# Performance work log

Measured on AMD Instinct MI355X. Metric: run time of the kernel, lower is better.

The kernel has to match this reference:

```python
import jax, jax.numpy as jnp
import numpy as np

HEAD_N = 16
EMBED_D = 1024
MASK_FILL = 1e-09  # source uses masked_fill(mask==0, 1e-09), NOT -inf


def setup_inputs() -> dict:
    key = jax.random.key(0)
    ks = jax.random.split(key, 8)
    B, S, D = 4, 4096, EMBED_D
    L = S // HEAD_N
    q = jax.random.normal(ks[0], (B, S, D), dtype=jnp.float32)
    k = jax.random.normal(ks[1], (B, S, D), dtype=jnp.float32)
    v = jax.random.normal(ks[2], (B, S, D), dtype=jnp.float32)
    mask = jax.random.randint(ks[3], (B, L, L), 0, 2, dtype=jnp.int32)
    scale = 0.02
    Wq = jax.random.normal(ks[4], (D, D), dtype=jnp.float32) * scale
    Wk = jax.random.normal(ks[5], (D, D), dtype=jnp.float32) * scale
    Wv = jax.random.normal(ks[6], (D, D), dtype=jnp.float32) * scale
    Wo = jax.random.normal(ks[7], (D, D), dtype=jnp.float32) * scale
    return {"q": q, "k": k, "v": v, "mask": mask, "Wq": Wq, "Wk": Wk, "Wv": Wv, "Wo": Wo}


def _split_heads(x, B):
    # Faithful to source bug: view(B, -1, head_n, embedding_d).transpose(1, 2)
    # -> splits the SEQUENCE dim by head_n; per-head dim stays EMBED_D.
    return x.reshape(B, -1, HEAD_N, EMBED_D).transpose(0, 2, 1, 3)  # [B,h,L,D]


def reference(q, k, v, mask, Wq, Wk, Wv, Wo):
    B, S, D = q.shape
    qh = _split_heads(q @ Wq, B)
    kh = _split_heads(k @ Wk, B)
    vh = _split_heads(v @ Wv, B)
    # score: [B, h, L, L], L = S // head_n
    score = jnp.einsum("bhld,bhmd->bhlm", qh, kh) / jnp.sqrt(jnp.float32(D))
    m = mask[:, None, :, :]  # unsqueeze(1) -> broadcast over heads
    score = jnp.where(m == 0, jnp.float32(MASK_FILL), score)
    att = jax.nn.softmax(score, axis=-1)  # dropout p=0.0 -> identity
    x = jnp.einsum("bhlm,bhmd->bhld", att, vh)  # [B,h,L,D]
    x = x.transpose(0, 2, 1, 3).reshape(B, S, D)
    return x @ Wo
```

## Files before the change

### kernel.cpp

```cpp
#include <hip/hip_runtime.h>
#include <hip/hip_bf16.h>

typedef __bf16 bf16x8 __attribute__((ext_vector_type(8)));
typedef float f32x4 __attribute__((ext_vector_type(4)));
typedef unsigned short ushort_t;
typedef unsigned int uint_t;

#define HN 16
#define LSEQ 256
#define DD 1024
#define BB 4
#define SS 4096
#define MROWS (BB * SS)
#define BHN (BB * HN)

__device__ __forceinline__ ushort_t f2bf(float f) {
  uint_t u = __builtin_bit_cast(uint_t, f);
  u += 0x7fffu + ((u >> 16) & 1u);
  return (ushort_t)(u >> 16);
}
__device__ __forceinline__ uint_t pk2(float lo, float hi) {
  return (uint_t)f2bf(lo) | ((uint_t)f2bf(hi) << 16);
}

__global__ __launch_bounds__(256) void cvt3(const float4* __restrict__ s0,
                                            const float4* __restrict__ s1,
                                            const float4* __restrict__ s2,
                                            uint4* __restrict__ out) {
  const int z = blockIdx.y;
  const float4* in = (z == 0) ? s0 : (z == 1) ? s1 : s2;
  const long i = (long)blockIdx.x * 256 + threadIdx.x;
  const float4 a = in[i * 2];
  const float4 b = in[i * 2 + 1];
  uint4 o;
  o.x = pk2(a.x, a.y);
  o.y = pk2(a.z, a.w);
  o.z = pk2(b.x, b.y);
  o.w = pk2(b.z, b.w);
  out[(long)z * 2097152 + i] = o;
}

__global__ __launch_bounds__(256) void transpose_w4(const float* __restrict__ W0,
                                                    const float* __restrict__ W1,
                                                    const float* __restrict__ W2,
                                                    const float* __restrict__ W3,
                                                    ushort_t* __restrict__ WT) {
  __shared__ float tile[32][33];
  const int z = blockIdx.z;
  const float* W = (z == 0) ? W0 : (z == 1) ? W1 : (z == 2) ? W2 : W3;
  ushort_t* dst = WT + (long)z * 1048576;
  const int tx = threadIdx.x, ty = threadIdx.y;
  const int bn = blockIdx.x * 32, bk = blockIdx.y * 32;
#pragma unroll
  for (int j = 0; j < 32; j += 8)
    tile[ty + j][tx] = W[(long)(bk + ty + j) * DD + bn + tx];
  __syncthreads();
#pragma unroll
  for (int j = 0; j < 32; j += 8)
    dst[(long)(bn + ty + j) * DD + bk + tx] = f2bf(tile[tx][ty + j]);
}

__global__ __launch_bounds__(256) void transpose_v(const ushort_t* __restrict__ vh,
                                                   ushort_t* __restrict__ vhT) {
  __shared__ ushort_t tile[32][33];
  const int tx = threadIdx.x, ty = threadIdx.y;
  const long zo = (long)blockIdx.z * (LSEQ * DD);
  const ushort_t* src = vh + zo;
  ushort_t* dst = vhT + zo;
  const int bd = blockIdx.x * 32;
  const int bl = blockIdx.y * 32;
#pragma unroll
  for (int j = 0; j < 32; j += 8)
    tile[ty + j][tx] = src[(long)(bl + ty + j) * DD + bd + tx];
  __syncthreads();
#pragma unroll
  for (int j = 0; j < 32; j += 8)
    dst[(long)(bd + ty + j) * LSEQ + bl + tx] = tile[tx][ty + j];
}

__global__ __launch_bounds__(256, 2) void score_sm(const ushort_t* __restrict__ qh,
                                                   const ushort_t* __restrict__ kh,
                                                   const int* __restrict__ mask,
                                                   ushort_t* __restrict__ att) {
  __shared__ char smemraw[81920];
  ushort_t* sA = (ushort_t*)smemraw;
  ushort_t* sB = (ushort_t*)(smemraw + 16384);
  float* Sf = (float*)smemraw;

  const int orig = blockIdx.x;
  const int wgid = (orig & 7) * 32 + (orig >> 3);
  const int bh = wgid >> 2, rb = wgid & 3;
  const int b = bh >> 4;
  const ushort_t* A = qh + ((long)bh * 256 + rb * 64) * 1024;
  const ushort_t* Bk = kh + (long)bh * 256 * 1024;

  const int t = threadIdx.x, lane = t & 63, wid = t >> 6;
  const int fr = lane & 15, q = lane >> 4;
  const int wc = wid * 64;
  const int sw0 = (q ^ (fr & 7)) * 8;
  const int sw1 = ((4 + q) ^ (fr & 7)) * 8;

  int srcAo[2], dstA[2], srcBo[8], dstB[8];
#pragma unroll
  for (int i = 0; i < 2; ++i) {
    const int c = i * 256 + t, row = c >> 3, gc = (c & 7) ^ (row & 7);
    srcAo[i] = row * 1024 + gc * 8;
    dstA[i] = (i * 256 + (t & 192)) * 8;
  }
#pragma unroll
  for (int i = 0; i < 8; ++i) {
    const int c = i * 256 + t, row = c >> 3, gc = (c & 7) ^ (row & 7);
    srcBo[i] = row * 1024 + gc * 8;
    dstB[i] = (i * 256 + (t & 192)) * 8;
  }

  auto stage = [&](int buf, int kt) {
    const int ko = kt * 64;
#pragma unroll
    for (int i = 0; i < 2; ++i)
      __builtin_amdgcn_global_load_lds(
          (const __attribute__((address_space(1))) void*)(A + srcAo[i] + ko),
          (__attribute__((address_space(3))) void*)(sA + buf * 4096 + dstA[i]), 16, 0, 0);
#pragma unroll
    for (int i = 0; i < 8; ++i)
      __builtin_amdgcn_global_load_lds(
          (const __attribute__((address_space(1))) void*)(Bk + srcBo[i] + ko),
          (__attribute__((address_space(3))) void*)(sB + buf * 16384 + dstB[i]), 16, 0, 0);
  };

  f32x4 acc[4][4];
#pragma unroll
  for (int m = 0; m < 4; ++m)
#pragma unroll
    for (int n = 0; n < 4; ++n) acc[m][n] = (f32x4){0.f, 0.f, 0.f, 0.f};

  stage(0, 0);
  __syncthreads();
  int cur = 0;
  for (int kt = 0; kt < 16; ++kt) {
    if (kt < 15) stage(cur ^ 1, kt + 1);
    bf16x8 af[4][2], bfv[4][2];
    const ushort_t* bA = sA + cur * 4096;
    const ushort_t* bB = sB + cur * 16384;
#pragma unroll
    for (int m = 0; m < 4; ++m) {
      af[m][0] = *(const bf16x8*)(bA + (m * 16 + fr) * 64 + sw0);
      af[m][1] = *(const bf16x8*)(bA + (m * 16 + fr) * 64 + sw1);
    }
#pragma unroll
    for (int n = 0; n < 4; ++n) {
      bfv[n][0] = *(const bf16x8*)(bB + (wc + n * 16 + fr) * 64 + sw0);
      bfv[n][1] = *(const bf16x8*)(bB + (wc + n * 16 + fr) * 64 + sw1);
    }
#pragma unroll
    for (int m = 0; m < 4; ++m)
#pragma unroll
      for (int n = 0; n < 4; ++n) {
        acc[m][n] = __builtin_amdgcn_mfma_f32_16x16x32_bf16(af[m][0], bfv[n][0], acc[m][n], 0, 0, 0);
        acc[m][n] = __builtin_amdgcn_mfma_f32_16x16x32_bf16(af[m][1], bfv[n][1], acc[m][n], 0, 0, 0);
      }
    __syncthreads();
    cur ^= 1;
  }

#pragma unroll
  for (int m = 0; m < 4; ++m)
#pragma unroll
    for (int n = 0; n < 4; ++n)
#pragma unroll
      for (int r = 0; r < 4; ++r)
        Sf[(m * 16 + q * 4 + r) * 256 + wc + n * 16 + fr] = acc[m][n][r];
  __syncthreads();

#pragma unroll 2
  for (int i = 0; i < 16; ++i) {
    const int row = wid * 16 + i;
    const int gl = rb * 64 + row;
    const f32x4 sv = *(const f32x4*)&Sf[row * 256 + lane * 4];
    const int4 mv = *(const int4*)&mask[((long)b * 256 + gl) * 256 + lane * 4];
    float s[4];
    s[0] = (mv.x == 0) ? 1e-9f : sv[0] * 0.03125f;
    s[1] = (mv.y == 0) ? 1e-9f : sv[1] * 0.03125f;
    s[2] = (mv.z == 0) ? 1e-9f : sv[2] * 0.03125f;
    s[3] = (mv.w == 0) ? 1e-9f : sv[3] * 0.03125f;
    float mx = fmaxf(fmaxf(s[0], s[1]), fmaxf(s[2], s[3]));
#pragma unroll
    for (int off = 32; off; off >>= 1) mx = fmaxf(mx, __shfl_xor(mx, off));
    float e[4], sum = 0.f;
#pragma unroll
    for (int j = 0; j < 4; ++j) {
      e[j] = __expf(s[j] - mx);
      sum += e[j];
    }
#pragma unroll
    for (int off = 32; off; off >>= 1) sum += __shfl_xor(sum, off);
    const float inv = 1.0f / sum;
    ushort4 o;
    o.x = f2bf(e[0] * inv);
    o.y = f2bf(e[1] * inv);
    o.z = f2bf(e[2] * inv);
    o.w = f2bf(e[3] * inv);
    *(ushort4*)&att[((long)bh * 256 + gl) * 256 + lane * 4] = o;
  }
}

__global__ __launch_bounds__(256, 2) void gemm_tn(const ushort_t* __restrict__ Ab,
                                                  const ushort_t* __restrict__ Btp,
                                                  void* __restrict__ Cp, int K, int ldA,
                                                  int ldB, int ldC, long batchA,
                                                  long batchB, long batchC) {
  __shared__ ushort_t smem[16384];
  ushort_t* sA = smem;
  ushort_t* sB = smem + 8192;

  const int bx = blockIdx.x, by = blockIdx.y, z = blockIdx.z;
  const int rowBase = by * 128;
  const int colBase = bx * 128;

  const int t = threadIdx.x;
  const int lane = t & 63;
  const int wid = t >> 6;
  const int wr = (wid >> 1) * 64;
  const int wc = (wid & 1) * 64;
  const int fr = lane & 15;
  const int fk = (lane >> 4) * 8;

  const ushort_t* Atile = Ab + batchA * z + (long)rowBase * ldA;
  const ushort_t* Btile = Btp + batchB * z + (long)colBase * ldB;

  f32x4 acc[4][4];
#pragma unroll
  for (int m = 0; m < 4; ++m)
#pragma unroll
    for (int n = 0; n < 4; ++n) acc[m][n] = (f32x4){0.f, 0.f, 0.f, 0.f};

  const int NT = K >> 5;

  auto stageAB = [&](int buf, int kt) {
    const long ko = (long)kt * 32;
#pragma unroll
    for (int i = 0; i < 2; ++i) {
      const int c = i * 256 + t;
      const int cw = i * 256 + (t & 192);
      __builtin_amdgcn_global_load_lds(
          (const __attribute__((address_space(1))) void*)(Atile + (long)(c >> 2) * ldA + ko +
                                                          (c & 3) * 8),
          (__attribute__((address_space(3))) void*)(sA + buf * 4096 + cw * 8), 16, 0, 0);
      __builtin_amdgcn_global_load_lds(
          (const __attribute__((address_space(1))) void*)(Btile + (long)(c >> 2) * ldB + ko +
                                                          (c & 3) * 8),
          (__attribute__((address_space(3))) void*)(sB + buf * 4096 + cw * 8), 16, 0, 0);
    }
  };

  stageAB(0, 0);
  __syncthreads();

  int cur = 0;
  for (int kt = 0; kt < NT; ++kt) {
    if (kt + 1 < NT) stageAB(cur ^ 1, kt + 1);

    bf16x8 af[4], bfv[4];
    const ushort_t* baseA = sA + cur * 4096 + fk;
    const ushort_t* baseB = sB + cur * 4096 + fk;
#pragma unroll
    for (int m = 0; m < 4; ++m) af[m] = *(const bf16x8*)(baseA + (wr + m * 16 + fr) * 32);
#pragma unroll
    for (int n = 0; n < 4; ++n) bfv[n] = *(const bf16x8*)(baseB + (wc + n * 16 + fr) * 32);

#pragma unroll
    for (int m = 0; m < 4; ++m)
#pragma unroll
      for (int n = 0; n < 4; ++n)
        acc[m][n] = __builtin_amdgcn_mfma_f32_16x16x32_bf16(af[m], bfv[n], acc[m][n], 0, 0, 0);

    __syncthreads();
    cur ^= 1;
  }

  const int rq = (lane >> 4) * 4;
#pragma unroll
  for (int m = 0; m < 4; ++m)
#pragma unroll
    for (int n = 0; n < 4; ++n)
#pragma unroll
      for (int r = 0; r < 4; ++r)
        smem[(wr + m * 16 + rq + r) * 128 + wc + n * 16 + fr] = f2bf(acc[m][n][r]);
  __syncthreads();
  ushort_t* Cb = (ushort_t*)Cp;
  const int c8 = (lane & 15) * 8;
#pragma unroll
  for (int i = 0; i < 8; ++i) {
    const int row = i * 16 + wid * 4 + (lane >> 4);
    const uint4 val = *(const uint4*)(smem + row * 128 + c8);
    const int l = rowBase + row;
    const int orow = ((z >> 4) << 12) + l * 16 + (z & 15);
    *(uint4*)(Cb + (long)orow * 1024 + colBase + c8) = val;
  }
}

#define SBAR() asm volatile("s_barrier" ::: "memory")
#define LGKM0() asm volatile("s_waitcnt lgkmcnt(0)" ::: "memory")
#define VM(N) asm volatile("s_waitcnt vmcnt(" #N ")" ::: "memory")

template <int SMODE>
__global__ __launch_bounds__(512, 1) void gemm256(const ushort_t* __restrict__ A0,
                                                  const ushort_t* __restrict__ A1,
                                                  const ushort_t* __restrict__ A2,
                                                  const ushort_t* __restrict__ Btp,
                                                  void* __restrict__ Cp, long bStrideZ,
                                                  long cStrideZ) {
  __shared__ ushort_t sm[65536];

  const int orig = blockIdx.x;
  const int cpx = (int)gridDim.x >> 3;
  const int wgid = (orig & 7) * cpx + (orig >> 3);
  const int z = wgid >> 8;
  const int tile = wgid & 255;
  const int by = tile >> 2, bx = tile & 3;
  const int rowBase = by * 256, colBase = bx * 256;

  const ushort_t* Ab = (z == 0) ? A0 : (z == 1) ? A1 : A2;
  const ushort_t* Bt = Btp + bStrideZ * z;

  const int t = threadIdx.x;
  const int lane = t & 63;
  const int wid = t >> 6;
  const int wm = wid >> 2;
  const int wn = wid & 3;
  const int fr = lane & 15;
  const int q = lane >> 4;

  const int sw0 = ((q ^ (fr & 7)) * 8);
  const int sw1 = (((4 + q) ^ (fr & 7)) * 8);
  const int aoff0 = fr * 64 + sw0;
  const int aoff1 = fr * 64 + sw1;
  const int bbase = ((wn & 1) * 64 + fr) * 64;
  const int boff0 = bbase + sw0;
  const int boff1 = bbase + sw1;

  const ushort_t* srcA[2][2];
  const ushort_t* srcB[2][2];
  int ldsoff[2];
#pragma unroll
  for (int i = 0; i < 2; ++i) {
    const int c = i * 512 + t;
    const int rowc = c >> 3;
    const int gc = (c & 7) ^ (rowc & 7);
    srcA[0][i] = Ab + (long)(rowBase + rowc) * 1024 + gc * 8;
    srcA[1][i] = Ab + (long)(rowBase + 128 + rowc) * 1024 + gc * 8;
    srcB[0][i] = Bt + (long)(colBase + rowc) * 1024 + gc * 8;
    srcB[1][i] = Bt + (long)(colBase + 128 + rowc) * 1024 + gc * 8;
    ldsoff[i] = (c & ~63) * 8;
  }

#define STAGE(kind, h, T)                                                                   \
  do {                                                                                      \
    ushort_t* _d = sm + ((kind) ? 32768 : 0) + ((T) & 1) * 16384 + (h) * 8192;              \
    const ushort_t* _s0 = ((kind) ? srcB[h][0] : srcA[h][0]) + (long)(T) * 64;              \
    __builtin_amdgcn_global_load_lds((const __attribute__((address_space(1))) void*)_s0,    \
                                     (__attribute__((address_space(3))) void*)(_d + ldsoff[0]), \
                                     16, 0, 0);                                             \
    const ushort_t* _s1 = ((kind) ? srcB[h][1] : srcA[h][1]) + (long)(T) * 64;              \
    __builtin_amdgcn_global_load_lds((const __attribute__((address_space(1))) void*)_s1,    \
                                     (__attribute__((address_space(3))) void*)(_d + ldsoff[1]), \
                                     16, 0, 0);                                             \
  } while (0)

  f32x4 acc[8][4];
#pragma unroll
  for (int m = 0; m < 8; ++m)
#pragma unroll
    for (int n = 0; n < 4; ++n) acc[m][n] = (f32x4){0.f, 0.f, 0.f, 0.f};

  bf16x8 af[4][2], bf0[2][2], bf1[2][2];

#define LDA4(dbuf, msub)                                                         \
  do {                                                                           \
    const ushort_t* _b = sm + (dbuf)*16384 + wm * 8192 + (msub)*4096;            \
    _Pragma("unroll") for (int m2 = 0; m2 < 4; ++m2) {                           \
      af[m2][0] = *(const bf16x8*)(_b + m2 * 1024 + aoff0);                      \
      af[m2][1] = *(const bf16x8*)(_b + m2 * 1024 + aoff1);                      \
    }                                                                            \
  } while (0)

#define LDB2(dbuf, nsub, bfv)                                                    \
  do {                                                                           \
    const ushort_t* _b = sm + 32768 + (dbuf)*16384 + (wn >> 1) * 8192 + (nsub)*2048; \
    _Pragma("unroll") for (int n2 = 0; n2 < 2; ++n2) {                           \
      bfv[n2][0] = *(const bf16x8*)(_b + n2 * 1024 + boff0);                     \
      bfv[n2][1] = *(const bf16x8*)(_b + n2 * 1024 + boff1);                     \
    }                                                                            \
  } while (0)

#define MMQ(msub, nsub, bfv)                                                     \
  do {                                                                           \
    _Pragma("unroll") for (int m2 = 0; m2 < 4; ++m2)                             \
        _Pragma("unroll") for (int n2 = 0; n2 < 2; ++n2) {                       \
      acc[(msub)*4 + m2][(nsub)*2 + n2] = __builtin_amdgcn_mfma_f32_16x16x32_bf16( \
          af[m2][0], bfv[n2][0], acc[(msub)*4 + m2][(nsub)*2 + n2], 0, 0, 0);    \
      acc[(msub)*4 + m2][(nsub)*2 + n2] = __builtin_amdgcn_mfma_f32_16x16x32_bf16( \
          af[m2][1], bfv[n2][1], acc[(msub)*4 + m2][(nsub)*2 + n2], 0, 0, 0);    \
    }                                                                            \
  } while (0)

#define PH_OPEN() SBAR(); LGKM0(); __builtin_amdgcn_s_setprio(1)
#define PH_CLOSE() __builtin_amdgcn_s_setprio(0); SBAR()

  const int NT = 16;
  const int NI = 8;

  STAGE(0, 0, 0);
  STAGE(0, 1, 0);
  STAGE(1, 0, 0);
  STAGE(1, 1, 0);
  STAGE(0, 0, 1);
  STAGE(0, 1, 1);
  STAGE(1, 0, 1);
  STAGE(1, 1, 1);
  VM(8);
  SBAR();

  for (int it = 0; it < NI - 1; ++it) {
    const int T0 = 2 * it;
    LDA4(0, 0);
    LDB2(0, 0, bf0);
    PH_OPEN(); MMQ(0, 0, bf0); PH_CLOSE();
    LDB2(0, 1, bf1);
    PH_OPEN(); MMQ(0, 1, bf1); PH_CLOSE();
    LDA4(0, 1);
    STAGE(1, 0, T0 + 2);
    STAGE(1, 1, T0 + 2);
    PH_OPEN(); MMQ(1, 1, bf1); PH_CLOSE();
    STAGE(0, 0, T0 + 2);
    STAGE(0, 1, T0 + 2);
    SBAR();
    __builtin_amdgcn_s_setprio(1);
    MMQ(1, 0, bf0);
    __builtin_amdgcn_s_setprio(0);
    VM(8);
    SBAR();
    LDA4(1, 0);
    LDB2(1, 0, bf0);
    PH_OPEN(); MMQ(0, 0, bf0); PH_CLOSE();
    LDB2(1, 1, bf1);
    PH_OPEN(); MMQ(0, 1, bf1); PH_CLOSE();
    LDA4(1, 1);
    STAGE(1, 0, T0 + 3);
    STAGE(1, 1, T0 + 3);
    PH_OPEN(); MMQ(1, 1, bf1); PH_CLOSE();
    STAGE(0, 0, T0 + 3);
    STAGE(0, 1, T0 + 3);
    SBAR();
    __builtin_amdgcn_s_setprio(1);
    MMQ(1, 0, bf0);
    __builtin_amdgcn_s_setprio(0);
    VM(8);
    SBAR();
  }

  {
    LDA4(0, 0);
    LDB2(0, 0, bf0);
    PH_OPEN(); MMQ(0, 0, bf0); PH_CLOSE();
    LDB2(0, 1, bf1);
    PH_OPEN(); MMQ(0, 1, bf1); PH_CLOSE();
    LDA4(0, 1);
    PH_OPEN(); MMQ(1, 1, bf1); PH_CLOSE();
    SBAR();
    __builtin_amdgcn_s_setprio(1);
    MMQ(1, 0, bf0);
    __builtin_amdgcn_s_setprio(0);
    VM(0);
    SBAR();
    LDA4(1, 0);
    LDB2(1, 0, bf0);
    PH_OPEN(); MMQ(0, 0, bf0); PH_CLOSE();
    LDB2(1, 1, bf1);
    PH_OPEN(); MMQ(0, 1, bf1); PH_CLOSE();
    LDA4(1, 1);
    PH_OPEN(); MMQ(1, 1, bf1); PH_CLOSE();
    SBAR();
    MMQ(1, 0, bf0);
    SBAR();
  }

  const int rq = q * 4;
  if constexpr (SMODE == 0) {
    float* Cf = (float*)Cp + cStrideZ * z;
#pragma unroll
    for (int m = 0; m < 8; ++m)
#pragma unroll
      for (int n = 0; n < 4; ++n)
#pragma unroll
        for (int r = 0; r < 4; ++r) {
          const int row = rowBase + wm * 128 + m * 16 + rq + r;
          const int col = colBase + wn * 64 + n * 16 + fr;
          Cf[(long)row * 1024 + col] = acc[m][n][r];
        }
  } else {
#pragma unroll
    for (int m = 0; m < 8; ++m)
#pragma unroll
      for (int n = 0; n < 4; ++n)
#pragma unroll
        for (int r = 0; r < 4; ++r) {
          const int row = wm * 128 + m * 16 + rq + r;
          const int col = wn * 64 + n * 16 + fr;
          sm[row * 256 + (((col >> 3) ^ (row & 7)) * 8) + (col & 7)] = f2bf(acc[m][n][r]);
        }
    __syncthreads();
    ushort_t* Cb = (ushort_t*)Cp + cStrideZ * z;
    const int cc = t & 31;
    const int r0 = t >> 5;
#pragma unroll
    for (int i = 0; i < 16; ++i) {
      const int row = r0 + i * 16;
      const uint4 val = *(const uint4*)(sm + row * 256 + ((cc ^ (row & 7)) * 8));
      const int grow = rowBase + row;
      const int b = grow >> 12;
      const int s = grow & 4095;
      const int orow = ((b << 4) + (s & 15)) * 256 + (s >> 4);
      *(uint4*)(Cb + (long)orow * 1024 + colBase + cc * 8) = val;
    }
  }
#undef STAGE
#undef LDA4
#undef LDB2
#undef MMQ
#undef PH_OPEN
#undef PH_CLOSE
}

extern "C" void kernel_launch(void* const* d_in, const int* in_sizes, int n_in,
                              void* d_out, int out_size, void* d_ws, size_t ws_size,
                              hipStream_t stream) {
  const float* q = (const float*)d_in[0];
  const float* k = (const float*)d_in[1];
  const float* v = (const float*)d_in[2];
  const int* mask = (const int*)d_in[3];
  const float* Wq = (const float*)d_in[4];
  const float* Wk = (const float*)d_in[5];
  const float* Wv = (const float*)d_in[6];
  const float* Wo = (const float*)d_in[7];
  float* out = (float*)d_out;

  char* ws = (char*)d_ws;
  const size_t MB = 1024 * 1024;
  ushort_t* WT = (ushort_t*)ws;
  const dim3 tb(32, 8);
  transpose_w4<<<dim3(32, 32, 4), tb, 0, stream>>>(Wq, Wk, Wv, Wo, WT);

  const bool big = ws_size >= (size_t)200 * MB;

  if (big) {
    ushort_t* qkvb = (ushort_t*)(ws + 8 * MB);
    ushort_t* qh = (ushort_t*)(ws + 104 * MB);
    ushort_t* kh = (ushort_t*)(ws + 136 * MB);
    ushort_t* vh = (ushort_t*)(ws + 168 * MB);
    ushort_t* vhT = (ushort_t*)(ws + 8 * MB);
    ushort_t* att = (ushort_t*)(ws + 40 * MB);
    ushort_t* x = (ushort_t*)(ws + 48 * MB);

    cvt3<<<dim3(8192, 3), 256, 0, stream>>>((const float4*)q, (const float4*)k,
                                            (const float4*)v, (uint4*)qkvb);
    gemm256<1><<<768, 512, 0, stream>>>(qkvb, qkvb + (size_t)16777216,
                                        qkvb + (size_t)33554432, WT, qh, 1 << 20,
                                        (long)16777216);
    transpose_v<<<dim3(32, 8, BHN), tb, 0, stream>>>(vh, vhT);
    score_sm<<<256, 256, 0, stream>>>(qh, kh, mask, att);
    gemm_tn<<<dim3(8, 2, BHN), 256, 0, stream>>>(att, vhT, x, 256, 256, 256, 1024,
                                                 (long)65536, (long)262144, 0);
    gemm256<0><<<256, 512, 0, stream>>>(x, x, x, WT + (size_t)3145728, out, 0, 0);
  } else {
    ushort_t* qb = (ushort_t*)(ws + 8 * MB);
    ushort_t* qh = (ushort_t*)(ws + 40 * MB);
    ushort_t* kh = (ushort_t*)(ws + 72 * MB);
    ushort_t* vh = (ushort_t*)(ws + 104 * MB);
    ushort_t* vhT = (ushort_t*)(ws + 136 * MB);
    ushort_t* att = (ushort_t*)(ws + 8 * MB);
    ushort_t* x = (ushort_t*)(ws + 16 * MB);

    cvt3<<<dim3(8192, 1), 256, 0, stream>>>((const float4*)q, (const float4*)q,
                                            (const float4*)q, (uint4*)qb);
    gemm256<1><<<256, 512, 0, stream>>>(qb, qb, qb, WT, qh, 0, 0);
    cvt3<<<dim3(8192, 1), 256, 0, stream>>>((const float4*)k, (const float4*)k,
                                            (const float4*)k, (uint4*)qb);
    gemm256<1><<<256, 512, 0, stream>>>(qb, qb, qb, WT + (size_t)1048576, kh, 0, 0);
    cvt3<<<dim3(8192, 1), 256, 0, stream>>>((const float4*)v, (const float4*)v,
                                            (const float4*)v, (uint4*)qb);
    gemm256<1><<<256, 512, 0, stream>>>(qb, qb, qb, WT + (size_t)2097152, vh, 0, 0);
    transpose_v<<<dim3(32, 8, BHN), tb, 0, stream>>>(vh, vhT);
    score_sm<<<256, 256, 0, stream>>>(qh, kh, mask, att);
    gemm_tn<<<dim3(8, 2, BHN), 256, 0, stream>>>(att, vhT, x, 256, 256, 256, 1024,
                                                 (long)65536, (long)262144, 0);
    gemm256<0><<<256, 512, 0, stream>>>(x, x, x, WT + (size_t)3145728, out, 0, 0);
  }
}
```

Baseline: 271.7 us.

## Fuse fp32-to-bf16 input conversion into the QKV projection GEMM

Removes the separate cvt3 pass that converted q, k and v to bf16. A new GEMM kernel instead loads fp32 A tiles straight into LDS and converts them to bf16 with v_cvt_pk_bf16_f32 while building MFMA fragments. This avoids writing and re-reading about 96MB of bf16 intermediates. In exchange, the A tiles take twice the LDS and global bandwidth per K step, the pipeline runs 32-wide K steps with a new schedule, and the small-workspace fallback path is dropped.

```diff
diff --git a/kernel.cpp b/kernel.cpp
--- a/kernel.cpp
+++ b/kernel.cpp
@@ -14,30 +14,18 @@
 #define MROWS (BB * SS)
 #define BHN (BB * HN)
 
+#define AS1 __attribute__((address_space(1)))
+#define AS3 __attribute__((address_space(3)))
+
 __device__ __forceinline__ ushort_t f2bf(float f) {
   uint_t u = __builtin_bit_cast(uint_t, f);
   u += 0x7fffu + ((u >> 16) & 1u);
   return (ushort_t)(u >> 16);
 }
-__device__ __forceinline__ uint_t pk2(float lo, float hi) {
-  return (uint_t)f2bf(lo) | ((uint_t)f2bf(hi) << 16);
-}
-
-__global__ __launch_bounds__(256) void cvt3(const float4* __restrict__ s0,
-                                            const float4* __restrict__ s1,
-                                            const float4* __restrict__ s2,
-                                            uint4* __restrict__ out) {
-  const int z = blockIdx.y;
-  const float4* in = (z == 0) ? s0 : (z == 1) ? s1 : s2;
-  const long i = (long)blockIdx.x * 256 + threadIdx.x;
-  const float4 a = in[i * 2];
-  const float4 b = in[i * 2 + 1];
-  uint4 o;
-  o.x = pk2(a.x, a.y);
-  o.y = pk2(a.z, a.w);
-  o.z = pk2(b.x, b.y);
-  o.w = pk2(b.z, b.w);
-  out[(long)z * 2097152 + i] = o;
+__device__ __forceinline__ uint_t cvtpk(float lo, float hi) {
+  uint_t r;
+  asm("v_cvt_pk_bf16_f32 %0, %1, %2" : "=v"(r) : "v"(lo), "v"(hi));
+  return r;
 }
 
 __global__ __launch_bounds__(256) void transpose_w4(const float* __restrict__ W0,
@@ -119,13 +107,13 @@
 #pragma unroll
     for (int i = 0; i < 2; ++i)
       __builtin_amdgcn_global_load_lds(
-          (const __attribute__((address_space(1))) void*)(A + srcAo[i] + ko),
-          (__attribute__((address_space(3))) void*)(sA + buf * 4096 + dstA[i]), 16, 0, 0);
+          (const AS1 void*)(A + srcAo[i] + ko),
+          (AS3 void*)(sA + buf * 4096 + dstA[i]), 16, 0, 0);
 #pragma unroll
     for (int i = 0; i < 8; ++i)
       __builtin_amdgcn_global_load_lds(
-          (const __attribute__((address_space(1))) void*)(Bk + srcBo[i] + ko),
-          (__attribute__((address_space(3))) void*)(sB + buf * 16384 + dstB[i]), 16, 0, 0);
+          (const AS1 void*)(Bk + srcBo[i] + ko),
+          (AS3 void*)(sB + buf * 16384 + dstB[i]), 16, 0, 0);
   };
 
   f32x4 acc[4][4];
@@ -243,13 +231,11 @@
       const int c = i * 256 + t;
       const int cw = i * 256 + (t & 192);
       __builtin_amdgcn_global_load_lds(
-          (const __attribute__((address_space(1))) void*)(Atile + (long)(c >> 2) * ldA + ko +
-                                                          (c & 3) * 8),
-          (__attribute__((address_space(3))) void*)(sA + buf * 4096 + cw * 8), 16, 0, 0);
+          (const AS1 void*)(Atile + (long)(c >> 2) * ldA + ko + (c & 3) * 8),
+          (AS3 void*)(sA + buf * 4096 + cw * 8), 16, 0, 0);
       __builtin_amdgcn_global_load_lds(
-          (const __attribute__((address_space(1))) void*)(Btile + (long)(c >> 2) * ldB + ko +
-                                                          (c & 3) * 8),
-          (__attribute__((address_space(3))) void*)(sB + buf * 4096 + cw * 8), 16, 0, 0);
+          (const AS1 void*)(Btile + (long)(c >> 2) * ldB + ko + (c & 3) * 8),
+          (AS3 void*)(sB + buf * 4096 + cw * 8), 16, 0, 0);
     }
   };
 
@@ -302,26 +288,23 @@
 #define SBAR() asm volatile("s_barrier" ::: "memory")
 #define LGKM0() asm volatile("s_waitcnt lgkmcnt(0)" ::: "memory")
 #define VM(N) asm volatile("s_waitcnt vmcnt(" #N ")" ::: "memory")
+#define PH_OPEN() SBAR(); LGKM0(); __builtin_amdgcn_s_setprio(1)
+#define PH_CLOSE() __builtin_amdgcn_s_setprio(0); SBAR()
 
 template <int SMODE>
 __global__ __launch_bounds__(512, 1) void gemm256(const ushort_t* __restrict__ A0,
-                                                  const ushort_t* __restrict__ A1,
-                                                  const ushort_t* __restrict__ A2,
                                                   const ushort_t* __restrict__ Btp,
-                                                  void* __restrict__ Cp, long bStrideZ,
-                                                  long cStrideZ) {
+                                                  void* __restrict__ Cp) {
   __shared__ ushort_t sm[65536];
 
   const int orig = blockIdx.x;
   const int cpx = (int)gridDim.x >> 3;
   const int wgid = (orig & 7) * cpx + (orig >> 3);
-  const int z = wgid >> 8;
-  const int tile = wgid & 255;
-  const int by = tile >> 2, bx = tile & 3;
+  const int by = wgid >> 2, bx = wgid & 3;
   const int rowBase = by * 256, colBase = bx * 256;
 
-  const ushort_t* Ab = (z == 0) ? A0 : (z == 1) ? A1 : A2;
-  const ushort_t* Bt = Btp + bStrideZ * z;
+  const ushort_t* Ab = A0;
+  const ushort_t* Bt = Btp;
 
   const int t = threadIdx.x;
   const int lane = t & 63;
@@ -358,13 +341,11 @@
   do {                                                                                      \
     ushort_t* _d = sm + ((kind) ? 32768 : 0) + ((T) & 1) * 16384 + (h) * 8192;              \
     const ushort_t* _s0 = ((kind) ? srcB[h][0] : srcA[h][0]) + (long)(T) * 64;              \
-    __builtin_amdgcn_global_load_lds((const __attribute__((address_space(1))) void*)_s0,    \
-                                     (__attribute__((address_space(3))) void*)(_d + ldsoff[0]), \
-                                     16, 0, 0);                                             \
+    __builtin_amdgcn_global_load_lds((const AS1 void*)_s0,                                  \
+                                     (AS3 void*)(_d + ldsoff[0]), 16, 0, 0);                \
     const ushort_t* _s1 = ((kind) ? srcB[h][1] : srcA[h][1]) + (long)(T) * 64;              \
-    __builtin_amdgcn_global_load_lds((const __attribute__((address_space(1))) void*)_s1,    \
-                                     (__attribute__((address_space(3))) void*)(_d + ldsoff[1]), \
-                                     16, 0, 0);                                             \
+    __builtin_amdgcn_global_load_lds((const AS1 void*)_s1,                                  \
+                                     (AS3 void*)(_d + ldsoff[1]), 16, 0, 0);                \
   } while (0)
 
   f32x4 acc[8][4];
@@ -403,9 +384,6 @@
           af[m2][1], bfv[n2][1], acc[(msub)*4 + m2][(nsub)*2 + n2], 0, 0, 0);    \
     }                                                                            \
   } while (0)
-
-#define PH_OPEN() SBAR(); LGKM0(); __builtin_amdgcn_s_setprio(1)
-#define PH_CLOSE() __builtin_amdgcn_s_setprio(0); SBAR()
 
   const int NT = 16;
   const int NI = 8;
@@ -487,7 +465,7 @@
 
   const int rq = q * 4;
   if constexpr (SMODE == 0) {
-    float* Cf = (float*)Cp + cStrideZ * z;
+    float* Cf = (float*)Cp;
 #pragma unroll
     for (int m = 0; m < 8; ++m)
 #pragma unroll
@@ -498,38 +476,230 @@
           const int col = colBase + wn * 64 + n * 16 + fr;
           Cf[(long)row * 1024 + col] = acc[m][n][r];
         }
-  } else {
-#pragma unroll
-    for (int m = 0; m < 8; ++m)
-#pragma unroll
-      for (int n = 0; n < 4; ++n)
-#pragma unroll
-        for (int r = 0; r < 4; ++r) {
-          const int row = wm * 128 + m * 16 + rq + r;
-          const int col = wn * 64 + n * 16 + fr;
-          sm[row * 256 + (((col >> 3) ^ (row & 7)) * 8) + (col & 7)] = f2bf(acc[m][n][r]);
-        }
-    __syncthreads();
-    ushort_t* Cb = (ushort_t*)Cp + cStrideZ * z;
-    const int cc = t & 31;
-    const int r0 = t >> 5;
-#pragma unroll
-    for (int i = 0; i < 16; ++i) {
-      const int row = r0 + i * 16;
-      const uint4 val = *(const uint4*)(sm + row * 256 + ((cc ^ (row & 7)) * 8));
-      const int grow = rowBase + row;
-      const int b = grow >> 12;
-      const int s = grow & 4095;
-      const int orow = ((b << 4) + (s & 15)) * 256 + (s >> 4);
-      *(uint4*)(Cb + (long)orow * 1024 + colBase + cc * 8) = val;
-    }
   }
 #undef STAGE
 #undef LDA4
 #undef LDB2
 #undef MMQ
-#undef PH_OPEN
-#undef PH_CLOSE
+}
+
+__global__ __launch_bounds__(512, 1) void gemm256f32a(const float* __restrict__ A0,
+                                                      const float* __restrict__ A1,
+                                                      const float* __restrict__ A2,
+                                                      const ushort_t* __restrict__ Btp,
+                                                      ushort_t* __restrict__ Cp) {
+  __shared__ ushort_t sm[65536];
+  char* smb = (char*)sm;
+
+  const int orig = blockIdx.x;
+  const int cpx = (int)gridDim.x >> 3;
+  const int wgid = (orig & 7) * cpx + (orig >> 3);
+  const int z = wgid >> 8;
+  const int tile = wgid & 255;
+  const int by = tile >> 2, bx = tile & 3;
+  const int rowBase = by * 256, colBase = bx * 256;
+
+  const float* Af = (z == 0) ? A0 : (z == 1) ? A1 : A2;
+  const ushort_t* Bt = Btp + (long)z * 1048576;
+
+  const int t = threadIdx.x;
+  const int lane = t & 63;
+  const int wid = t >> 6;
+  const int wm = wid >> 2;
+  const int wn = wid & 3;
+  const int fr = lane & 15;
+  const int q = lane >> 4;
+
+  const int sA0 = ((2 * q) ^ (fr & 7)) * 16;
+  const int sA1 = ((2 * q + 1) ^ (fr & 7)) * 16;
+  const int sB0 = ((q) ^ (fr & 7)) * 8;
+  const int sB1 = ((4 + q) ^ (fr & 7)) * 8;
+
+  const float* srcA[4];
+  int ldsAu[4];
+  const ushort_t* srcBt[4];
+  int ldsBu[4];
+#pragma unroll
+  for (int i = 0; i < 4; ++i) {
+    const int cA = i * 512 + t;
+    const int rA = cA >> 3;
+    const int gA = (cA & 7) ^ (rA & 7);
+    srcA[i] = Af + (long)(rowBase + rA) * 1024 + gA * 4;
+    ldsAu[i] = (cA & ~63) * 16;
+    const int cB = i * 512 + t;
+    const int rB = cB >> 3;
+    const int gB = (cB & 7) ^ (rB & 7);
+    srcBt[i] = Bt + (long)(colBase + rB) * 1024 + gB * 8;
+    ldsBu[i] = (cB & ~63) * 8;
+  }
+
+#define SAF4(T, d)                                                                          \
+  do {                                                                                      \
+    _Pragma("unroll") for (int _i = 0; _i < 4; ++_i)                                        \
+        __builtin_amdgcn_global_load_lds((const AS1 void*)(srcA[_i] + (long)(T) * 32),      \
+                                         (AS3 void*)(smb + (d)*32768 + ldsAu[_i]), 16, 0, 0); \
+  } while (0)
+
+#define SBF(b, bb)                                                                          \
+  do {                                                                                      \
+    _Pragma("unroll") for (int _i = 0; _i < 4; ++_i)                                        \
+        __builtin_amdgcn_global_load_lds((const AS1 void*)(srcBt[_i] + (long)(b) * 64),     \
+                                         (AS3 void*)(sm + 32768 + (bb)*16384 + ldsBu[_i]),  \
+                                         16, 0, 0);                                         \
+  } while (0)
+
+  f32x4 acc[8][4];
+#pragma unroll
+  for (int m = 0; m < 8; ++m)
+#pragma unroll
+    for (int n = 0; n < 4; ++n) acc[m][n] = (f32x4){0.f, 0.f, 0.f, 0.f};
+
+  bf16x8 af[4], bf0[2], bf1[2];
+
+#define LDA4F(d, msub)                                                                      \
+  do {                                                                                      \
+    _Pragma("unroll") for (int m2 = 0; m2 < 4; ++m2) {                                      \
+      const char* _p = smb + (d)*32768 + (wm * 128 + (msub)*64 + m2 * 16 + fr) * 128;       \
+      const float4 _u = *(const float4*)(_p + sA0);                                         \
+      const float4 _v = *(const float4*)(_p + sA1);                                         \
+      uint4 _w;                                                                             \
+      _w.x = cvtpk(_u.x, _u.y);                                                             \
+      _w.y = cvtpk(_u.z, _u.w);                                                             \
+      _w.z = cvtpk(_v.x, _v.y);                                                             \
+      _w.w = cvtpk(_v.z, _v.w);                                                             \
+      af[m2] = __builtin_bit_cast(bf16x8, _w);                                              \
+    }                                                                                       \
+  } while (0)
+
+#define LDB2F(bb, SBOFF, nsub, bfv)                                                         \
+  do {                                                                                      \
+    _Pragma("unroll") for (int n2 = 0; n2 < 2; ++n2) {                                      \
+      const int _row = (wn >> 1) * 128 + (wn & 1) * 64 + (nsub)*32 + n2 * 16 + fr;          \
+      bfv[n2] = *(const bf16x8*)(sm + 32768 + (bb)*16384 + _row * 64 + (SBOFF));            \
+    }                                                                                       \
+  } while (0)
+
+#define MMQF(msub, nsub, bfv)                                                               \
+  do {                                                                                      \
+    _Pragma("unroll") for (int m2 = 0; m2 < 4; ++m2)                                        \
+        _Pragma("unroll") for (int n2 = 0; n2 < 2; ++n2) acc[(msub)*4 + m2][(nsub)*2 + n2] = \
+        __builtin_amdgcn_mfma_f32_16x16x32_bf16(af[m2], bfv[n2],                            \
+                                                acc[(msub)*4 + m2][(nsub)*2 + n2], 0, 0, 0); \
+  } while (0)
+
+#define ITER_E(T, d, bb, bdst)                                                              \
+  do {                                                                                      \
+    LDA4F(d, 0);                                                                            \
+    LDB2F(bb, sB0, 0, bf0);                                                                 \
+    SBF(((T) >> 1) + 1, bdst);                                                              \
+    PH_OPEN(); MMQF(0, 0, bf0); PH_CLOSE();                                                 \
+    LDB2F(bb, sB0, 1, bf1);                                                                 \
+    PH_OPEN(); MMQF(0, 1, bf1); PH_CLOSE();                                                 \
+    LDA4F(d, 1);                                                                            \
+    PH_OPEN(); MMQF(1, 1, bf1); PH_CLOSE();                                                 \
+    SAF4((T) + 2, d);                                                                       \
+    SBAR();                                                                                 \
+    __builtin_amdgcn_s_setprio(1);                                                          \
+    MMQF(1, 0, bf0);                                                                        \
+    __builtin_amdgcn_s_setprio(0);                                                          \
+    VM(8);                                                                                  \
+    SBAR();                                                                                 \
+  } while (0)
+
+#define ITER_O(T, d, bb)                                                                    \
+  do {                                                                                      \
+    LDA4F(d, 0);                                                                            \
+    LDB2F(bb, sB1, 0, bf0);                                                                 \
+    PH_OPEN(); MMQF(0, 0, bf0); PH_CLOSE();                                                 \
+    LDB2F(bb, sB1, 1, bf1);                                                                 \
+    PH_OPEN(); MMQF(0, 1, bf1); PH_CLOSE();                                                 \
+    LDA4F(d, 1);                                                                            \
+    PH_OPEN(); MMQF(1, 1, bf1); PH_CLOSE();                                                 \
+    SAF4((T) + 2, d);                                                                       \
+    SBAR();                                                                                 \
+    __builtin_amdgcn_s_setprio(1);                                                          \
+    MMQF(1, 0, bf0);                                                                        \
+    __builtin_amdgcn_s_setprio(0);                                                          \
+    VM(4);                                                                                  \
+    SBAR();                                                                                 \
+  } while (0)
+
+  SBF(0, 0);
+  SAF4(0, 0);
+  SAF4(1, 1);
+  VM(4);
+  SBAR();
+
+  for (int u = 0; u < 7; ++u) {
+    const int T0 = 4 * u;
+    ITER_E(T0, 0, 0, 1);
+    ITER_O(T0 + 1, 1, 0);
+    ITER_E(T0 + 2, 0, 1, 0);
+    ITER_O(T0 + 3, 1, 1);
+  }
+  ITER_E(28, 0, 0, 1);
+  ITER_O(29, 1, 0);
+
+  {
+    LDA4F(0, 0);
+    LDB2F(1, sB0, 0, bf0);
+    PH_OPEN(); MMQF(0, 0, bf0); PH_CLOSE();
+    LDB2F(1, sB0, 1, bf1);
+    PH_OPEN(); MMQF(0, 1, bf1); PH_CLOSE();
+    LDA4F(0, 1);
+    PH_OPEN(); MMQF(1, 1, bf1); PH_CLOSE();
+    SBAR();
+    __builtin_amdgcn_s_setprio(1);
+    MMQF(1, 0, bf0);
+    __builtin_amdgcn_s_setprio(0);
+    VM(0);
+    SBAR();
+  }
+  {
+    LDA4F(1, 0);
+    LDB2F(1, sB1, 0, bf0);
+    PH_OPEN(); MMQF(0, 0, bf0); PH_CLOSE();
+    LDB2F(1, sB1, 1, bf1);
+    PH_OPEN(); MMQF(0, 1, bf1); PH_CLOSE();
+    LDA4F(1, 1);
+    PH_OPEN(); MMQF(1, 1, bf1); PH_CLOSE();
+    SBAR();
+    MMQF(1, 0, bf0);
+    SBAR();
+  }
+
+  const int rq = q * 4;
+#pragma unroll
+  for (int m = 0; m < 8; ++m)
+#pragma unroll
+    for (int n = 0; n < 4; ++n)
+#pragma unroll
+      for (int r = 0; r < 4; ++r) {
+        const int row = wm * 128 + m * 16 + rq + r;
+        const int col = wn * 64 + n * 16 + fr;
+        sm[row * 256 + (((col >> 3) ^ (row & 7)) * 8) + (col & 7)] = f2bf(acc[m][n][r]);
+      }
+  __syncthreads();
+  ushort_t* Cb = Cp + (long)z * 16777216;
+  const int cc = t & 31;
+  const int r0 = t >> 5;
+#pragma unroll
+  for (int i = 0; i < 16; ++i) {
+    const int row = r0 + i * 16;
+    const uint4 val = *(const uint4*)(sm + row * 256 + ((cc ^ (row & 7)) * 8));
+    const int grow = rowBase + row;
+    const int b = grow >> 12;
+    const int s = grow & 4095;
+    const int orow = ((b << 4) + (s & 15)) * 256 + (s >> 4);
+    *(uint4*)(Cb + (long)orow * 1024 + colBase + cc * 8) = val;
+  }
+#undef SAF4
+#undef SBF
+#undef LDA4F
+#undef LDB2F
+#undef MMQF
+#undef ITER_E
+#undef ITER_O
 }
 
 extern "C" void kernel_launch(void* const* d_in, const int* in_sizes, int n_in,
@@ -548,52 +718,21 @@
   char* ws = (char*)d_ws;
   const size_t MB = 1024 * 1024;
   ushort_t* WT = (ushort_t*)ws;
+  ushort_t* qh = (ushort_t*)(ws + 8 * MB);
+  ushort_t* kh = (ushort_t*)(ws + 40 * MB);
+  ushort_t* vh = (ushort_t*)(ws + 72 * MB);
+  ushort_t* vhT = (ushort_t*)(ws + 104 * MB);
+  ushort_t* att = (ushort_t*)(ws + 136 * MB);
+  ushort_t* x = (ushort_t*)(ws + 144 * MB);
+
   const dim3 tb(32, 8);
   transpose_w4<<<dim3(32, 32, 4), tb, 0, stream>>>(Wq, Wk, Wv, Wo, WT);
 
-  const bool big = ws_size >= (size_t)200 * MB;
-
-  if (big) {
-    ushort_t* qkvb = (ushort_t*)(ws + 8 * MB);
-    ushort_t* qh = (ushort_t*)(ws + 104 * MB);
-    ushort_t* kh = (ushort_t*)(ws + 136 * MB);
-    ushort_t* vh = (ushort_t*)(ws + 168 * MB);
-    ushort_t* vhT = (ushort_t*)(ws + 8 * MB);
-    ushort_t* att = (ushort_t*)(ws + 40 * MB);
-    ushort_t* x = (ushort_t*)(ws + 48 * MB);
-
-    cvt3<<<dim3(8192, 3), 256, 0, stream>>>((const float4*)q, (const float4*)k,
-                                            (const float4*)v, (uint4*)qkvb);
-    gemm256<1><<<768, 512, 0, stream>>>(qkvb, qkvb + (size_t)16777216,
-                                        qkvb + (size_t)33554432, WT, qh, 1 << 20,
-                                        (long)16777216);
-    transpose_v<<<dim3(32, 8, BHN), tb, 0, stream>>>(vh, vhT);
-    score_sm<<<256, 256, 0, stream>>>(qh, kh, mask, att);
-    gemm_tn<<<dim3(8, 2, BHN), 256, 0, stream>>>(att, vhT, x, 256, 256, 256, 1024,
-                                                 (long)65536, (long)262144, 0);
-    gemm256<0><<<256, 512, 0, stream>>>(x, x, x, WT + (size_t)3145728, out, 0, 0);
-  } else {
-    ushort_t* qb = (ushort_t*)(ws + 8 * MB);
-    ushort_t* qh = (ushort_t*)(ws + 40 * MB);
-    ushort_t* kh = (ushort_t*)(ws + 72 * MB);
-    ushort_t* vh = (ushort_t*)(ws + 104 * MB);
-    ushort_t* vhT = (ushort_t*)(ws + 136 * MB);
-    ushort_t* att = (ushort_t*)(ws + 8 * MB);
-    ushort_t* x = (ushort_t*)(ws + 16 * MB);
-
-    cvt3<<<dim3(8192, 1), 256, 0, stream>>>((const float4*)q, (const float4*)q,
-                                            (const float4*)q, (uint4*)qb);
-    gemm256<1><<<256, 512, 0, stream>>>(qb, qb, qb, WT, qh, 0, 0);
-    cvt3<<<dim3(8192, 1), 256, 0, stream>>>((const float4*)k, (const float4*)k,
-                                            (const float4*)k, (uint4*)qb);
-    gemm256<1><<<256, 512, 0, stream>>>(qb, qb, qb, WT + (size_t)1048576, kh, 0, 0);
-    cvt3<<<dim3(8192, 1), 256, 0, stream>>>((const float4*)v, (const float4*)v,
-                                            (const float4*)v, (uint4*)qb);
-    gemm256<1><<<256, 512, 0, stream>>>(qb, qb, qb, WT + (size_t)2097152, vh, 0, 0);
-    transpose_v<<<dim3(32, 8, BHN), tb, 0, stream>>>(vh, vhT);
-    score_sm<<<256, 256, 0, stream>>>(qh, kh, mask, att);
-    gemm_tn<<<dim3(8, 2, BHN), 256, 0, stream>>>(att, vhT, x, 256, 256, 256, 1024,
-                                                 (long)65536, (long)262144, 0);
-    gemm256<0><<<256, 512, 0, stream>>>(x, x, x, WT + (size_t)3145728, out, 0, 0);
-  }
-}
+  gemm256f32a<<<768, 512, 0, stream>>>(q, k, v, WT, qh);
+
+  transpose_v<<<dim3(32, 8, BHN), tb, 0, stream>>>(vh, vhT);
+  score_sm<<<256, 256, 0, stream>>>(qh, kh, mask, att);
+  gemm_tn<<<dim3(8, 2, BHN), 256, 0, stream>>>(att, vhT, x, 256, 256, 256, 1024,
+                                               (long)65536, (long)262144, 0);
+  gemm256<0><<<256, 512, 0, stream>>>(x, WT + (size_t)3145728, out);
+}
```

Result: slower. 334.3 us (+23.1%).

## Fuse V transpose into projection GEMM epilogue with k-blocked layout

Applied to the files above, without the earlier changes.

Removes the separate transpose_v kernel. The V projection GEMM epilogue now writes V directly in a transposed, k-chunked layout of 16-element groups, and gemm_tn's B-loader computes addresses into that layout. This saves one kernel launch and a full read and write of the V tensor, in exchange for a more scattered epilogue store with scalar LDS gathers.

```diff
diff --git a/kernel.cpp b/kernel.cpp
--- a/kernel.cpp
+++ b/kernel.cpp
@@ -13,6 +13,9 @@
 #define SS 4096
 #define MROWS (BB * SS)
 #define BHN (BB * HN)
+
+#define AS1 __attribute__((address_space(1)))
+#define AS3 __attribute__((address_space(3)))
 
 __device__ __forceinline__ ushort_t f2bf(float f) {
   uint_t u = __builtin_bit_cast(uint_t, f);
@@ -60,24 +63,6 @@
     dst[(long)(bn + ty + j) * DD + bk + tx] = f2bf(tile[tx][ty + j]);
 }
 
-__global__ __launch_bounds__(256) void transpose_v(const ushort_t* __restrict__ vh,
-                                                   ushort_t* __restrict__ vhT) {
-  __shared__ ushort_t tile[32][33];
-  const int tx = threadIdx.x, ty = threadIdx.y;
-  const long zo = (long)blockIdx.z * (LSEQ * DD);
-  const ushort_t* src = vh + zo;
-  ushort_t* dst = vhT + zo;
-  const int bd = blockIdx.x * 32;
-  const int bl = blockIdx.y * 32;
-#pragma unroll
-  for (int j = 0; j < 32; j += 8)
-    tile[ty + j][tx] = src[(long)(bl + ty + j) * DD + bd + tx];
-  __syncthreads();
-#pragma unroll
-  for (int j = 0; j < 32; j += 8)
-    dst[(long)(bd + ty + j) * LSEQ + bl + tx] = tile[tx][ty + j];
-}
-
 __global__ __launch_bounds__(256, 2) void score_sm(const ushort_t* __restrict__ qh,
                                                    const ushort_t* __restrict__ kh,
                                                    const int* __restrict__ mask,
@@ -119,13 +104,13 @@
 #pragma unroll
     for (int i = 0; i < 2; ++i)
       __builtin_amdgcn_global_load_lds(
-          (const __attribute__((address_space(1))) void*)(A + srcAo[i] + ko),
-          (__attribute__((address_space(3))) void*)(sA + buf * 4096 + dstA[i]), 16, 0, 0);
+          (const AS1 void*)(A + srcAo[i] + ko),
+          (AS3 void*)(sA + buf * 4096 + dstA[i]), 16, 0, 0);
 #pragma unroll
     for (int i = 0; i < 8; ++i)
       __builtin_amdgcn_global_load_lds(
-          (const __attribute__((address_space(1))) void*)(Bk + srcBo[i] + ko),
-          (__attribute__((address_space(3))) void*)(sB + buf * 16384 + dstB[i]), 16, 0, 0);
+          (const AS1 void*)(Bk + srcBo[i] + ko),
+          (AS3 void*)(sB + buf * 16384 + dstB[i]), 16, 0, 0);
   };
 
   f32x4 acc[4][4];
@@ -207,8 +192,7 @@
 __global__ __launch_bounds__(256, 2) void gemm_tn(const ushort_t* __restrict__ Ab,
                                                   const ushort_t* __restrict__ Btp,
                                                   void* __restrict__ Cp, int K, int ldA,
-                                                  int ldB, int ldC, long batchA,
-                                                  long batchB, long batchC) {
+                                                  int ldC, long batchA, long batchB) {
   __shared__ ushort_t smem[16384];
   ushort_t* sA = smem;
   ushort_t* sB = smem + 8192;
@@ -226,7 +210,15 @@
   const int fk = (lane >> 4) * 8;
 
   const ushort_t* Atile = Ab + batchA * z + (long)rowBase * ldA;
-  const ushort_t* Btile = Btp + batchB * z + (long)colBase * ldB;
+  const ushort_t* Btile = Btp + batchB * z;
+
+  int sBstat[2];
+#pragma unroll
+  for (int i = 0; i < 2; ++i) {
+    const int c = i * 256 + t;
+    const int x8 = (c & 3) * 8;
+    sBstat[i] = (x8 >> 4) * 16384 + (colBase + (c >> 2)) * 16 + (x8 & 15);
+  }
 
   f32x4 acc[4][4];
 #pragma unroll
@@ -243,13 +235,11 @@
       const int c = i * 256 + t;
       const int cw = i * 256 + (t & 192);
       __builtin_amdgcn_global_load_lds(
-          (const __attribute__((address_space(1))) void*)(Atile + (long)(c >> 2) * ldA + ko +
-                                                          (c & 3) * 8),
-          (__attribute__((address_space(3))) void*)(sA + buf * 4096 + cw * 8), 16, 0, 0);
+          (const AS1 void*)(Atile + (long)(c >> 2) * ldA + ko + (c & 3) * 8),
+          (AS3 void*)(sA + buf * 4096 + cw * 8), 16, 0, 0);
       __builtin_amdgcn_global_load_lds(
-          (const __attribute__((address_space(1))) void*)(Btile + (long)(c >> 2) * ldB + ko +
-                                                          (c & 3) * 8),
-          (__attribute__((address_space(3))) void*)(sB + buf * 4096 + cw * 8), 16, 0, 0);
+          (const AS1 void*)(Btile + sBstat[i] + (long)kt * 32768),
+          (AS3 void*)(sB + buf * 4096 + cw * 8), 16, 0, 0);
     }
   };
 
@@ -302,6 +292,8 @@
 #define SBAR() asm volatile("s_barrier" ::: "memory")
 #define LGKM0() asm volatile("s_waitcnt lgkmcnt(0)" ::: "memory")
 #define VM(N) asm volatile("s_waitcnt vmcnt(" #N ")" ::: "memory")
+#define PH_OPEN() SBAR(); LGKM0(); __builtin_amdgcn_s_setprio(1)
+#define PH_CLOSE() __builtin_amdgcn_s_setprio(0); SBAR()
 
 template <int SMODE>
 __global__ __launch_bounds__(512, 1) void gemm256(const ushort_t* __restrict__ A0,
@@ -309,7 +301,7 @@
                                                   const ushort_t* __restrict__ A2,
                                                   const ushort_t* __restrict__ Btp,
                                                   void* __restrict__ Cp, long bStrideZ,
-                                                  long cStrideZ) {
+                                                  long cStrideZ, int vzsel) {
   __shared__ ushort_t sm[65536];
 
   const int orig = blockIdx.x;
@@ -358,13 +350,11 @@
   do {                                                                                      \
     ushort_t* _d = sm + ((kind) ? 32768 : 0) + ((T) & 1) * 16384 + (h) * 8192;              \
     const ushort_t* _s0 = ((kind) ? srcB[h][0] : srcA[h][0]) + (long)(T) * 64;              \
-    __builtin_amdgcn_global_load_lds((const __attribute__((address_space(1))) void*)_s0,    \
-                                     (__attribute__((address_space(3))) void*)(_d + ldsoff[0]), \
-                                     16, 0, 0);                                             \
+    __builtin_amdgcn_global_load_lds((const AS1 void*)_s0,                                  \
+                                     (AS3 void*)(_d + ldsoff[0]), 16, 0, 0);                \
     const ushort_t* _s1 = ((kind) ? srcB[h][1] : srcA[h][1]) + (long)(T) * 64;              \
-    __builtin_amdgcn_global_load_lds((const __attribute__((address_space(1))) void*)_s1,    \
-                                     (__attribute__((address_space(3))) void*)(_d + ldsoff[1]), \
-                                     16, 0, 0);                                             \
+    __builtin_amdgcn_global_load_lds((const AS1 void*)_s1,                                  \
+                                     (AS3 void*)(_d + ldsoff[1]), 16, 0, 0);                \
   } while (0)
 
   f32x4 acc[8][4];
@@ -403,9 +393,6 @@
           af[m2][1], bfv[n2][1], acc[(msub)*4 + m2][(nsub)*2 + n2], 0, 0, 0);    \
     }                                                                            \
   } while (0)
-
-#define PH_OPEN() SBAR(); LGKM0(); __builtin_amdgcn_s_setprio(1)
-#define PH_CLOSE() __builtin_amdgcn_s_setprio(0); SBAR()
 
   const int NT = 16;
   const int NI = 8;
@@ -511,25 +498,47 @@
         }
     __syncthreads();
     ushort_t* Cb = (ushort_t*)Cp + cStrideZ * z;
-    const int cc = t & 31;
-    const int r0 = t >> 5;
-#pragma unroll
-    for (int i = 0; i < 16; ++i) {
-      const int row = r0 + i * 16;
-      const uint4 val = *(const uint4*)(sm + row * 256 + ((cc ^ (row & 7)) * 8));
-      const int grow = rowBase + row;
-      const int b = grow >> 12;
-      const int s = grow & 4095;
-      const int orow = ((b << 4) + (s & 15)) * 256 + (s >> 4);
-      *(uint4*)(Cb + (long)orow * 1024 + colBase + cc * 8) = val;
+    if (z != vzsel) {
+      const int cc = t & 31;
+      const int r0 = t >> 5;
+#pragma unroll
+      for (int i = 0; i < 16; ++i) {
+        const int row = r0 + i * 16;
+        const uint4 val = *(const uint4*)(sm + row * 256 + ((cc ^ (row & 7)) * 8));
+        const int grow = rowBase + row;
+        const int b = grow >> 12;
+        const int s = grow & 4095;
+        const int orow = ((b << 4) + (s & 15)) * 256 + (s >> 4);
+        *(uint4*)(Cb + (long)orow * 1024 + colBase + cc * 8) = val;
+      }
+    } else {
+      const int bq = rowBase >> 12;
+      const int lblk = (rowBase & 4095) >> 8;
+      ushort_t* base0 = Cb + (long)lblk * 16384;
+#pragma unroll
+      for (int i = 0; i < 8; ++i) {
+        const int cid = i * 512 + t;
+        const int d = cid & 255;
+        const int h = cid >> 8;
+        uint_t w[8];
+#pragma unroll
+        for (int j = 0; j < 8; ++j) {
+          const int r0 = (2 * j) * 16 + h;
+          const int r1 = (2 * j + 1) * 16 + h;
+          const ushort_t v0 = sm[r0 * 256 + (((d >> 3) ^ (r0 & 7)) * 8) + (d & 7)];
+          const ushort_t v1 = sm[r1 * 256 + (((d >> 3) ^ (r1 & 7)) * 8) + (d & 7)];
+          w[j] = (uint_t)v0 | ((uint_t)v1 << 16);
+        }
+        ushort_t* dst = base0 + (long)(bq * 16 + h) * 262144 + (colBase + d) * 16;
+        *(uint4*)dst = make_uint4(w[0], w[1], w[2], w[3]);
+        *(uint4*)(dst + 8) = make_uint4(w[4], w[5], w[6], w[7]);
+      }
     }
   }
 #undef STAGE
 #undef LDA4
 #undef LDB2
 #undef MMQ
-#undef PH_OPEN
-#undef PH_CLOSE
 }
 
 extern "C" void kernel_launch(void* const* d_in, const int* in_sizes, int n_in,
@@ -557,8 +566,7 @@
     ushort_t* qkvb = (ushort_t*)(ws + 8 * MB);
     ushort_t* qh = (ushort_t*)(ws + 104 * MB);
     ushort_t* kh = (ushort_t*)(ws + 136 * MB);
-    ushort_t* vh = (ushort_t*)(ws + 168 * MB);
-    ushort_t* vhT = (ushort_t*)(ws + 8 * MB);
+    ushort_t* vhT2 = (ushort_t*)(ws + 168 * MB);
     ushort_t* att = (ushort_t*)(ws + 40 * MB);
     ushort_t* x = (ushort_t*)(ws + 48 * MB);
 
@@ -566,34 +574,31 @@
                                             (const float4*)v, (uint4*)qkvb);
     gemm256<1><<<768, 512, 0, stream>>>(qkvb, qkvb + (size_t)16777216,
                                         qkvb + (size_t)33554432, WT, qh, 1 << 20,
-                                        (long)16777216);
-    transpose_v<<<dim3(32, 8, BHN), tb, 0, stream>>>(vh, vhT);
+                                        (long)16777216, 2);
     score_sm<<<256, 256, 0, stream>>>(qh, kh, mask, att);
-    gemm_tn<<<dim3(8, 2, BHN), 256, 0, stream>>>(att, vhT, x, 256, 256, 256, 1024,
-                                                 (long)65536, (long)262144, 0);
-    gemm256<0><<<256, 512, 0, stream>>>(x, x, x, WT + (size_t)3145728, out, 0, 0);
+    gemm_tn<<<dim3(8, 2, BHN), 256, 0, stream>>>(att, vhT2, x, 256, 256, 1024,
+                                                 (long)65536, (long)262144);
+    gemm256<0><<<256, 512, 0, stream>>>(x, x, x, WT + (size_t)3145728, out, 0, 0, -1);
   } else {
     ushort_t* qb = (ushort_t*)(ws + 8 * MB);
     ushort_t* qh = (ushort_t*)(ws + 40 * MB);
     ushort_t* kh = (ushort_t*)(ws + 72 * MB);
-    ushort_t* vh = (ushort_t*)(ws + 104 * MB);
-    ushort_t* vhT = (ushort_t*)(ws + 136 * MB);
+    ushort_t* vhT2 = (ushort_t*)(ws + 104 * MB);
     ushort_t* att = (ushort_t*)(ws + 8 * MB);
     ushort_t* x = (ushort_t*)(ws + 16 * MB);
 
     cvt3<<<dim3(8192, 1), 256, 0, stream>>>((const float4*)q, (const float4*)q,
                                             (const float4*)q, (uint4*)qb);
-    gemm256<1><<<256, 512, 0, stream>>>(qb, qb, qb, WT, qh, 0, 0);
+    gemm256<1><<<256, 512, 0, stream>>>(qb, qb, qb, WT, qh, 0, 0, -1);
     cvt3<<<dim3(8192, 1), 256, 0, stream>>>((const float4*)k, (const float4*)k,
                                             (const float4*)k, (uint4*)qb);
-    gemm256<1><<<256, 512, 0, stream>>>(qb, qb, qb, WT + (size_t)1048576, kh, 0, 0);
+    gemm256<1><<<256, 512, 0, stream>>>(qb, qb, qb, WT + (size_t)1048576, kh, 0, 0, -1);
     cvt3<<<dim3(8192, 1), 256, 0, stream>>>((const float4*)v, (const float4*)v,
                                             (const float4*)v, (uint4*)qb);
-    gemm256<1><<<256, 512, 0, stream>>>(qb, qb, qb, WT + (size_t)2097152, vh, 0, 0);
-    transpose_v<<<dim3(32, 8, BHN), tb, 0, stream>>>(vh, vhT);
+    gemm256<1><<<256, 512, 0, stream>>>(qb, qb, qb, WT + (size_t)2097152, vhT2, 0, 0, 0);
     score_sm<<<256, 256, 0, stream>>>(qh, kh, mask, att);
-    gemm_tn<<<dim3(8, 2, BHN), 256, 0, stream>>>(att, vhT, x, 256, 256, 256, 1024,
-                                                 (long)65536, (long)262144, 0);
-    gemm256<0><<<256, 512, 0, stream>>>(x, x, x, WT + (size_t)3145728, out, 0, 0);
-  }
-}
+    gemm_tn<<<dim3(8, 2, BHN), 256, 0, stream>>>(att, vhT2, x, 256, 256, 1024,
+                                                 (long)65536, (long)262144);
+    gemm256<0><<<256, 512, 0, stream>>>(x, x, x, WT + (size_t)3145728, out, 0, 0, -1);
+  }
+}
```

Measured after the change: 257.9 us. 5.1% less time.
